# Kernel tuning notes

Hardware: AMD Instinct MI355X
Metric: run time of the kernel (lower is better)

## Reference

```python
import jax, jax.numpy as jnp
import numpy as np

NUM_HEADS = 8


def setup_inputs() -> dict:
    key = jax.random.key(0)
    ks = jax.random.split(key, 8)
    B, S, D = 2, 4096, 512
    # Linear weights init uniform(-0.1, 0.1), no bias; stored as [in, out]
    u = lambda k, shp: jax.random.uniform(k, shp, jnp.float32, -0.1, 0.1)
    return {
        "query_antecedent": jax.random.normal(ks[0], (B, S, D), jnp.float32),
        "memory_antecedent": jax.random.normal(ks[1], (B, S, D), jnp.float32),
        "bias": jax.random.normal(ks[2], (1, S, S), jnp.float32),
        "Wq": u(ks[3], (D, D)),
        "Wk": u(ks[4], (D, D)),
        "Wv": u(ks[5], (D, D)),
        "Wo": u(ks[6], (D, D)),
    }


def reference(query_antecedent, memory_antecedent, bias, Wq, Wk, Wv, Wo):
    B, S, D = query_antecedent.shape
    H = NUM_HEADS
    hd = D // H
    scale = hd ** (-0.5)
    q = (query_antecedent @ Wq) * scale              # [B,S,D]
    k = memory_antecedent @ Wk                       # [B,S,D]
    v = memory_antecedent @ Wv                       # [B,S,D]
    q = q.reshape(B, S, H, hd)
    k = k.reshape(B, S, H, hd)
    v = v.reshape(B, S, H, hd)
    # per-head logits with shared bias (broadcast over batch and heads)
    logits = jnp.einsum("bqhd,bkhd->bhqk", q, k) + bias[:, None, :, :]
    weights = jax.nn.softmax(logits, axis=-1)        # [B,H,S,S]
    out = jnp.einsum("bhqk,bkhd->bqhd", weights, v).reshape(B, S, D)
    return out @ Wo
```

## Files before the change

### kernel.cpp

```cpp
#include <hip/hip_runtime.h>
#include <hip/hip_bf16.h>

typedef __attribute__((ext_vector_type(8))) __bf16 bf16x8;
typedef __attribute__((ext_vector_type(4))) __bf16 bf16x4;
typedef __attribute__((ext_vector_type(4))) float f32x4;
typedef __attribute__((ext_vector_type(2))) unsigned u32x2;
typedef __attribute__((ext_vector_type(4))) unsigned u32x4;

#define LOG2E 1.4426950408889634f
#define FIXED_M 16.0f

static __device__ __forceinline__ f32x4 mfma16(bf16x8 a, bf16x8 b, f32x4 c) {
  return __builtin_amdgcn_mfma_f32_16x16x32_bf16(a, b, c, 0, 0, 0);
}

static __device__ __forceinline__ void gload_lds16(const void* g, void* l) {
  __builtin_amdgcn_global_load_lds(
      (const __attribute__((address_space(1))) unsigned int*)g,
      (__attribute__((address_space(3))) unsigned int*)l, 16, 0, 0);
}

__global__ __launch_bounds__(256) void k_cvt(const float* __restrict__ in,
                                             __bf16* __restrict__ out, int n4) {
  for (int i = blockIdx.x * blockDim.x + threadIdx.x; i < n4;
       i += gridDim.x * blockDim.x) {
    float4 v = reinterpret_cast<const float4*>(in)[i];
    bf16x4 o = {(__bf16)v.x, (__bf16)v.y, (__bf16)v.z, (__bf16)v.w};
    reinterpret_cast<bf16x4*>(out)[i] = o;
  }
}

__global__ __launch_bounds__(256) void k_wt(const float* __restrict__ W,
                                            __bf16* __restrict__ Wt) {
  __shared__ float tile[64][65];
  int bx = blockIdx.x;
  int by = blockIdx.y;
  int tid = threadIdx.x;
#pragma unroll
  for (int p = 0; p < 16; p++) {
    int idx = p * 256 + tid;
    int r = idx >> 6, c = idx & 63;
    tile[r][c] = W[(size_t)(by * 64 + r) * 512 + bx * 64 + c];
  }
  __syncthreads();
#pragma unroll
  for (int p = 0; p < 16; p++) {
    int idx = p * 256 + tid;
    int rn = idx >> 6, ck = idx & 63;
    Wt[(size_t)(bx * 64 + rn) * 512 + by * 64 + ck] = (__bf16)tile[ck][rn];
  }
}

template <int OUT_MODE>
__global__ __launch_bounds__(256) void k_gemm(const __bf16* __restrict__ A,
                                              const __bf16* __restrict__ Bt,
                                              void* __restrict__ Cout,
                                              float scale) {
  constexpr bool SWAP = (OUT_MODE != 2);
  __shared__ __bf16 As[128][72];
  __shared__ __bf16 Bs[64][72];
  const int tid = threadIdx.x;
  const int wid = tid >> 6, lane = tid & 63;
  const int g = lane >> 4, c = lane & 15;
  const int m0 = blockIdx.x * 128, n0 = blockIdx.y * 64;
  const int wr = wid >> 1, wc = wid & 1;

  f32x4 acc[4][2];
#pragma unroll
  for (int i = 0; i < 4; i++)
#pragma unroll
    for (int j = 0; j < 2; j++) acc[i][j] = (f32x4){0.f, 0.f, 0.f, 0.f};

  for (int k0 = 0; k0 < 512; k0 += 64) {
#pragma unroll
    for (int q = 0; q < 4; q++) {
      int idx = (q * 256 + tid) * 8;
      int r = idx >> 6, cc = idx & 63;
      bf16x8 v = *reinterpret_cast<const bf16x8*>(A + (size_t)(m0 + r) * 512 + k0 + cc);
      *reinterpret_cast<bf16x8*>(&As[r][cc]) = v;
    }
#pragma unroll
    for (int q = 0; q < 2; q++) {
      int idx = (q * 256 + tid) * 8;
      int r = idx >> 6, cc = idx & 63;
      bf16x8 v = *reinterpret_cast<const bf16x8*>(Bt + (size_t)(n0 + r) * 512 + k0 + cc);
      *reinterpret_cast<bf16x8*>(&Bs[r][cc]) = v;
    }
    __syncthreads();
#pragma unroll
    for (int kk = 0; kk < 2; kk++) {
      bf16x8 bfrag[2];
#pragma unroll
      for (int nf = 0; nf < 2; nf++)
        bfrag[nf] = *reinterpret_cast<const bf16x8*>(&Bs[wc * 32 + nf * 16 + c][kk * 32 + g * 8]);
#pragma unroll
      for (int mf = 0; mf < 4; mf++) {
        bf16x8 afrag = *reinterpret_cast<const bf16x8*>(&As[wr * 64 + mf * 16 + c][kk * 32 + g * 8]);
#pragma unroll
        for (int nf = 0; nf < 2; nf++)
          acc[mf][nf] = SWAP ? mfma16(bfrag[nf], afrag, acc[mf][nf])
                             : mfma16(afrag, bfrag[nf], acc[mf][nf]);
      }
    }
    __syncthreads();
  }
#pragma unroll
  for (int mf = 0; mf < 4; mf++)
#pragma unroll
    for (int nf = 0; nf < 2; nf++) {
      if (OUT_MODE == 0) {
        int mm = m0 + wr * 64 + mf * 16 + c;
        int nnb = n0 + wc * 32 + nf * 16 + g * 4;
        int b = mm >> 12, s = mm & 4095, h = nnb >> 6, d = nnb & 63;
        bf16x4 ov = {(__bf16)(acc[mf][nf][0] * scale), (__bf16)(acc[mf][nf][1] * scale),
                     (__bf16)(acc[mf][nf][2] * scale), (__bf16)(acc[mf][nf][3] * scale)};
        *reinterpret_cast<bf16x4*>((__bf16*)Cout + ((((size_t)b * 8 + h) * 4096) + s) * 64 + d) = ov;
      } else if (OUT_MODE == 1) {
        int mm = m0 + wr * 64 + mf * 16 + c;
        int nnb = n0 + wc * 32 + nf * 16 + g * 4;
        f32x4 ov = acc[mf][nf] * scale;
        *reinterpret_cast<f32x4*>((float*)Cout + (size_t)mm * 512 + nnb) = ov;
      } else {
        int mmb = m0 + wr * 64 + mf * 16 + g * 4;
        int nn = n0 + wc * 32 + nf * 16 + c;
        int b = mmb >> 12, s = mmb & 4095, h = nn >> 6, d = nn & 63;
        bf16x4 ov = {(__bf16)(acc[mf][nf][0] * scale), (__bf16)(acc[mf][nf][1] * scale),
                     (__bf16)(acc[mf][nf][2] * scale), (__bf16)(acc[mf][nf][3] * scale)};
        *reinterpret_cast<bf16x4*>((__bf16*)Cout + (((size_t)b * 8 + h) * 64 + d) * 4096 + s) = ov;
      }
    }
}

__global__ __launch_bounds__(256, 2) void k_attn(const __bf16* __restrict__ Q,
                                                 const __bf16* __restrict__ K,
                                                 const __bf16* __restrict__ Vt,
                                                 const float* __restrict__ bias,
                                                 __bf16* __restrict__ Out) {
  __shared__ __bf16 KVs[2][2][2][64][64];

  const int id = blockIdx.x;
  const int qb = ((id >> 6) << 3) | (id & 7);
  const int h = (id >> 3) & 7;
  const int tid = threadIdx.x, wid = tid >> 6, lane = tid & 63;
  const int g = lane >> 4, c = lane & 15;
  const int swz = (c & 7) << 4;
  const char* KbP[2] = {(const char*)(K + (size_t)h * 4096 * 64),
                        (const char*)(K + (size_t)(8 + h) * 4096 * 64)};
  const char* VbP[2] = {(const char*)(Vt + (size_t)h * 64 * 4096),
                        (const char*)(Vt + (size_t)(8 + h) * 64 * 4096)};
  const int q0 = qb * 64 + wid * 16;
  const int myq = q0 + c;

  auto stage = [&](int db, int chunk) {
    const int bt = wid >> 1, reg = wid & 1;
    char* dst0 = (char*)&KVs[db][bt][reg][0][0];
#pragma unroll
    for (int j = 0; j < 8; j++) {
      int Lp = j * 1024 + lane * 16;
      int L = Lp ^ (((Lp >> 7) & 7) << 4);
      const char* src = (reg == 0)
          ? KbP[bt] + (size_t)chunk * 8192 + L
          : VbP[bt] + (size_t)(L >> 7) * 8192 + (size_t)chunk * 128 + (L & 127);
      gload_lds16(src, dst0 + j * 1024);
    }
  };

  const float* brow = bias + (size_t)myq * 4096;

#define LOADB(dst, chunk)                                                      \
  {                                                                            \
    _Pragma("unroll") for (int f = 0; f < 4; f++) dst[f] =                     \
        *reinterpret_cast<const f32x4*>(brow + (chunk) * 64 + f * 16 + g * 4); \
  }

  bf16x8 qa[2][2];
  {
    const __bf16* Qh0 = Q + (size_t)h * 4096 * 64;
    const __bf16* Qh1 = Q + (size_t)(8 + h) * 4096 * 64;
    qa[0][0] = *reinterpret_cast<const bf16x8*>(Qh0 + (size_t)myq * 64 + g * 8);
    qa[0][1] = *reinterpret_cast<const bf16x8*>(Qh0 + (size_t)myq * 64 + 32 + g * 8);
    qa[1][0] = *reinterpret_cast<const bf16x8*>(Qh1 + (size_t)myq * 64 + g * 8);
    qa[1][1] = *reinterpret_cast<const bf16x8*>(Qh1 + (size_t)myq * 64 + 32 + g * 8);
  }

  f32x4 lacc[2];
  lacc[0] = (f32x4){0.f, 0.f, 0.f, 0.f};
  lacc[1] = (f32x4){0.f, 0.f, 0.f, 0.f};
  f32x4 o[2][4];
#pragma unroll
  for (int bt = 0; bt < 2; bt++)
#pragma unroll
    for (int f = 0; f < 4; f++) o[bt][f] = (f32x4){0.f, 0.f, 0.f, 0.f};

  f32x4 bA[4], bB[4];
  const float NM = -FIXED_M * LOG2E;

  auto process = [&](int db, f32x4 (&bv)[4]) {
    asm volatile("s_waitcnt vmcnt(12)" ::: "memory");
    __builtin_amdgcn_s_barrier();
#pragma unroll
    for (int bt = 0; bt < 2; bt++) {
      const char* Kl = (const char*)&KVs[db][bt][0][0][0];
      const char* Vl = (const char*)&KVs[db][bt][1][0][0];
      f32x4 st[4];
      __builtin_amdgcn_s_setprio(1);
#pragma unroll
      for (int f = 0; f < 4; f++) {
        const char* rb = Kl + (f * 16 + c) * 128;
        bf16x8 k0 = *reinterpret_cast<const bf16x8*>(rb + ((g * 16) ^ swz));
        bf16x8 k1 = *reinterpret_cast<const bf16x8*>(rb + ((64 + g * 16) ^ swz));
        st[f] = mfma16(k1, qa[bt][1], mfma16(k0, qa[bt][0], bv[f]));
      }
      __builtin_amdgcn_s_setprio(0);
      bf16x8 vf[2][4];
#pragma unroll
      for (int kk = 0; kk < 2; kk++)
#pragma unroll
        for (int fd = 0; fd < 4; fd++) {
          const char* rb = Vl + (fd * 16 + c) * 128;
          u32x2 lo = *reinterpret_cast<const u32x2*>(rb + ((kk * 64 + g * 8) ^ swz));
          u32x2 hi = *reinterpret_cast<const u32x2*>(rb + ((kk * 64 + 32 + g * 8) ^ swz));
          u32x4 w = {lo[0], lo[1], hi[0], hi[1]};
          vf[kk][fd] = __builtin_bit_cast(bf16x8, w);
        }
#pragma unroll
      for (int f = 0; f < 4; f++) {
#pragma unroll
        for (int r = 0; r < 4; r++)
          st[f][r] = __builtin_exp2f(__builtin_fmaf(st[f][r], LOG2E, NM));
        lacc[bt] += st[f];
      }
      __builtin_amdgcn_s_setprio(1);
#pragma unroll
      for (int kk = 0; kk < 2; kk++) {
        bf16x8 pf = {(__bf16)st[2 * kk][0],     (__bf16)st[2 * kk][1],
                     (__bf16)st[2 * kk][2],     (__bf16)st[2 * kk][3],
                     (__bf16)st[2 * kk + 1][0], (__bf16)st[2 * kk + 1][1],
                     (__bf16)st[2 * kk + 1][2], (__bf16)st[2 * kk + 1][3]};
#pragma unroll
        for (int fd = 0; fd < 4; fd++)
          o[bt][fd] = mfma16(vf[kk][fd], pf, o[bt][fd]);
      }
      __builtin_amdgcn_s_setprio(0);
    }
    __builtin_amdgcn_s_barrier();
  };

  stage(0, 0);
  asm volatile("" ::: "memory");
  stage(1, 1);
  asm volatile("" ::: "memory");
  LOADB(bA, 0);
  asm volatile("" ::: "memory");
  LOADB(bB, 1);
  asm volatile("" ::: "memory");

  for (int t = 0; t < 64; t += 2) {
    process(0, bA);
    stage(0, (t + 2) & 63);
    asm volatile("" ::: "memory");
    LOADB(bA, ((t + 2) & 63));
    asm volatile("" ::: "memory");
    process(1, bB);
    stage(1, (t + 3) & 63);
    asm volatile("" ::: "memory");
    LOADB(bB, ((t + 3) & 63));
    asm volatile("" ::: "memory");
  }

#pragma unroll
  for (int bt = 0; bt < 2; bt++) {
    float l = lacc[bt][0] + lacc[bt][1] + lacc[bt][2] + lacc[bt][3];
    l += __shfl_xor(l, 16);
    l += __shfl_xor(l, 32);
    float inv = 1.f / l;
    __bf16* Orow = Out + ((size_t)bt * 4096 + myq) * 512 + h * 64;
#pragma unroll
    for (int fd = 0; fd < 4; fd++) {
      bf16x4 ov = {(__bf16)(o[bt][fd][0] * inv), (__bf16)(o[bt][fd][1] * inv),
                   (__bf16)(o[bt][fd][2] * inv), (__bf16)(o[bt][fd][3] * inv)};
      *reinterpret_cast<bf16x4*>(Orow + fd * 16 + g * 4) = ov;
    }
  }
#undef LOADB
}

extern "C" void kernel_launch(void* const* d_in, const int* in_sizes, int n_in,
                              void* d_out, int out_size, void* d_ws, size_t ws_size,
                              hipStream_t stream) {
  const float* xq = (const float*)d_in[0];
  const float* xm = (const float*)d_in[1];
  const float* bias = (const float*)d_in[2];
  const float* Wq = (const float*)d_in[3];
  const float* Wk = (const float*)d_in[4];
  const float* Wv = (const float*)d_in[5];
  const float* Wo = (const float*)d_in[6];

  const size_t MB = 1024 * 1024;
  char* ws = (char*)d_ws;
  __bf16* xq_b = (__bf16*)(ws + 0);
  __bf16* xm_b = (__bf16*)(ws + 8 * MB);
  __bf16* wqt = (__bf16*)(ws + 16 * MB);
  __bf16* wkt = (__bf16*)(ws + 16 * MB + 524288);
  __bf16* wvt = (__bf16*)(ws + 17 * MB);
  __bf16* wot = (__bf16*)(ws + 17 * MB + 524288);
  __bf16* Qb = (__bf16*)(ws + 18 * MB);
  __bf16* Kb = (__bf16*)(ws + 26 * MB);
  __bf16* AOb = (__bf16*)(ws + 34 * MB);
  __bf16* Vtb = (__bf16*)(ws + 42 * MB);
  if (ws_size < 50 * MB) return;

  const int n4 = 8192 * 512 / 4;
  k_cvt<<<2048, 256, 0, stream>>>(xq, xq_b, n4);
  k_cvt<<<2048, 256, 0, stream>>>(xm, xm_b, n4);
  k_wt<<<dim3(8, 8), 256, 0, stream>>>(Wq, wqt);
  k_wt<<<dim3(8, 8), 256, 0, stream>>>(Wk, wkt);
  k_wt<<<dim3(8, 8), 256, 0, stream>>>(Wv, wvt);
  k_wt<<<dim3(8, 8), 256, 0, stream>>>(Wo, wot);

  k_gemm<0><<<dim3(64, 8), 256, 0, stream>>>(xq_b, wqt, Qb, 0.125f);
  k_gemm<0><<<dim3(64, 8), 256, 0, stream>>>(xm_b, wkt, Kb, 1.0f);
  k_gemm<2><<<dim3(64, 8), 256, 0, stream>>>(xm_b, wvt, Vtb, 1.0f);

  k_attn<<<512, 256, 0, stream>>>(Qb, Kb, Vtb, bias, AOb);

  k_gemm<1><<<dim3(64, 8), 256, 0, stream>>>(AOb, wot, d_out, 1.0f);
}
```

Before: 229.3 us.

## Software-pipeline PV MFMAs one tile behind QK and exp

Restructures the attention inner loop so the P·V MFMAs for the previous KV tile are issued together with the current tile's QK MFMAs, while exp and bf16 packing of the current scores happen afterward. P fragments and V fragments are carried across iterations in registers, with a prologue without PV and an epilogue that flushes the last PV. The goal is to overlap transcendental/VALU work with matrix-core work instead of serializing them. The cost is more live registers (vfP holds 16 bf16x8 values), which risks spills or lower occupancy.

Result: slower. 276.4 us (+20.5%).

```diff
diff --git a/kernel.cpp b/kernel.cpp
--- a/kernel.cpp
+++ b/kernel.cpp
@@ -192,27 +192,57 @@
 #pragma unroll
     for (int f = 0; f < 4; f++) o[bt][f] = (f32x4){0.f, 0.f, 0.f, 0.f};
 
+  bf16x8 pfP[2][2];
+  bf16x8 vfP[2][2][4];
+
   f32x4 bA[4], bB[4];
   const float NM = -FIXED_M * LOG2E;
 
-  auto process = [&](int db, f32x4 (&bv)[4]) {
+  auto process = [&](int db, f32x4 (&bv)[4], bool do_pv) {
     asm volatile("s_waitcnt vmcnt(12)" ::: "memory");
     __builtin_amdgcn_s_barrier();
+    f32x4 st[2][4];
+    __builtin_amdgcn_s_setprio(1);
 #pragma unroll
     for (int bt = 0; bt < 2; bt++) {
       const char* Kl = (const char*)&KVs[db][bt][0][0][0];
-      const char* Vl = (const char*)&KVs[db][bt][1][0][0];
-      f32x4 st[4];
-      __builtin_amdgcn_s_setprio(1);
 #pragma unroll
       for (int f = 0; f < 4; f++) {
         const char* rb = Kl + (f * 16 + c) * 128;
         bf16x8 k0 = *reinterpret_cast<const bf16x8*>(rb + ((g * 16) ^ swz));
         bf16x8 k1 = *reinterpret_cast<const bf16x8*>(rb + ((64 + g * 16) ^ swz));
-        st[f] = mfma16(k1, qa[bt][1], mfma16(k0, qa[bt][0], bv[f]));
+        st[bt][f] = mfma16(k1, qa[bt][1], mfma16(k0, qa[bt][0], bv[f]));
       }
-      __builtin_amdgcn_s_setprio(0);
-      bf16x8 vf[2][4];
+    }
+    if (do_pv) {
+#pragma unroll
+      for (int bt = 0; bt < 2; bt++)
+#pragma unroll
+        for (int kk = 0; kk < 2; kk++)
+#pragma unroll
+          for (int fd = 0; fd < 4; fd++)
+            o[bt][fd] = mfma16(vfP[bt][kk][fd], pfP[bt][kk], o[bt][fd]);
+    }
+    __builtin_amdgcn_s_setprio(0);
+#pragma unroll
+    for (int bt = 0; bt < 2; bt++) {
+#pragma unroll
+      for (int f = 0; f < 4; f++) {
+#pragma unroll
+        for (int r = 0; r < 4; r++)
+          st[bt][f][r] = __builtin_exp2f(__builtin_fmaf(st[bt][f][r], LOG2E, NM));
+        lacc[bt] += st[bt][f];
+      }
+#pragma unroll
+      for (int kk = 0; kk < 2; kk++)
+        pfP[bt][kk] = (bf16x8){(__bf16)st[bt][2 * kk][0],     (__bf16)st[bt][2 * kk][1],
+                               (__bf16)st[bt][2 * kk][2],     (__bf16)st[bt][2 * kk][3],
+                               (__bf16)st[bt][2 * kk + 1][0], (__bf16)st[bt][2 * kk + 1][1],
+                               (__bf16)st[bt][2 * kk + 1][2], (__bf16)st[bt][2 * kk + 1][3]};
+    }
+#pragma unroll
+    for (int bt = 0; bt < 2; bt++) {
+      const char* Vl = (const char*)&KVs[db][bt][1][0][0];
 #pragma unroll
       for (int kk = 0; kk < 2; kk++)
 #pragma unroll
@@ -221,27 +251,8 @@
           u32x2 lo = *reinterpret_cast<const u32x2*>(rb + ((kk * 64 + g * 8) ^ swz));
           u32x2 hi = *reinterpret_cast<const u32x2*>(rb + ((kk * 64 + 32 + g * 8) ^ swz));
           u32x4 w = {lo[0], lo[1], hi[0], hi[1]};
-          vf[kk][fd] = __builtin_bit_cast(bf16x8, w);
+          vfP[bt][kk][fd] = __builtin_bit_cast(bf16x8, w);
         }
-#pragma unroll
-      for (int f = 0; f < 4; f++) {
-#pragma unroll
-        for (int r = 0; r < 4; r++)
-          st[f][r] = __builtin_exp2f(__builtin_fmaf(st[f][r], LOG2E, NM));
-        lacc[bt] += st[f];
-      }
-      __builtin_amdgcn_s_setprio(1);
-#pragma unroll
-      for (int kk = 0; kk < 2; kk++) {
-        bf16x8 pf = {(__bf16)st[2 * kk][0],     (__bf16)st[2 * kk][1],
-                     (__bf16)st[2 * kk][2],     (__bf16)st[2 * kk][3],
-                     (__bf16)st[2 * kk + 1][0], (__bf16)st[2 * kk + 1][1],
-                     (__bf16)st[2 * kk + 1][2], (__bf16)st[2 * kk + 1][3]};
-#pragma unroll
-        for (int fd = 0; fd < 4; fd++)
-          o[bt][fd] = mfma16(vf[kk][fd], pf, o[bt][fd]);
-      }
-      __builtin_amdgcn_s_setprio(0);
     }
     __builtin_amdgcn_s_barrier();
   };
@@ -255,18 +266,37 @@
   LOADB(bB, 1);
   asm volatile("" ::: "memory");
 
-  for (int t = 0; t < 64; t += 2) {
-    process(0, bA);
+  process(0, bA, false);
+  stage(0, 2);
+  asm volatile("" ::: "memory");
+  LOADB(bA, 2);
+  asm volatile("" ::: "memory");
+  process(1, bB, true);
+  stage(1, 3);
+  asm volatile("" ::: "memory");
+  LOADB(bB, 3);
+  asm volatile("" ::: "memory");
+
+  for (int t = 2; t < 64; t += 2) {
+    process(0, bA, true);
     stage(0, (t + 2) & 63);
     asm volatile("" ::: "memory");
     LOADB(bA, ((t + 2) & 63));
     asm volatile("" ::: "memory");
-    process(1, bB);
+    process(1, bB, true);
     stage(1, (t + 3) & 63);
     asm volatile("" ::: "memory");
     LOADB(bB, ((t + 3) & 63));
     asm volatile("" ::: "memory");
   }
+
+#pragma unroll
+  for (int bt = 0; bt < 2; bt++)
+#pragma unroll
+    for (int kk = 0; kk < 2; kk++)
+#pragma unroll
+      for (int fd = 0; fd < 4; fd++)
+        o[bt][fd] = mfma16(vfP[bt][kk][fd], pfP[bt][kk], o[bt][fd]);
 
 #pragma unroll
   for (int bt = 0; bt < 2; bt++) {
```
